# Performance work log

Measured on AMD Instinct MI355X. Metric: run time of the kernel, lower is better.

The kernel has to match this reference:

```python
import jax, jax.numpy as jnp
import numpy as np

KH, KW = 3, 3
C_OUT = 32


def setup_inputs() -> dict:
    key = jax.random.key(0)
    k1, k2, k3 = jax.random.split(key, 3)
    B, H, W, C_IN = 32, 128, 128, 32
    P_DIM = 128
    X = jax.random.normal(k1, (B, H, W, C_IN), dtype=jnp.float32)
    P = jax.random.normal(k2, (B, P_DIM), dtype=jnp.float32)
    # hypernetwork Dense weight: p_dim -> kh*kw*c_in*c_out (no bias, no activation)
    dense_w = jax.random.normal(k3, (P_DIM, KH * KW * C_IN * C_OUT), dtype=jnp.float32) * 0.05
    return {"X": X, "P": P, "dense_w": dense_w}


def _conv_one(x, w):
    # x: [H, W, c_in], w: [kh, kw, c_in, c_out] -> [H, W, c_out], SAME padding, stride 1
    y = jax.lax.conv_general_dilated(
        x[None], w, window_strides=(1, 1), padding="SAME",
        dimension_numbers=("NHWC", "HWIO", "NHWC"))
    return y[0]


def reference(X, P, dense_w):
    B = X.shape[0]
    c_in = X.shape[-1]
    # hypernetwork: per-sample conv kernels
    A = P @ dense_w                              # [B, kh*kw*c_in*c_out]
    Wk = A.reshape(B, KH, KW, c_in, C_OUT)       # [B, kh, kw, c_in, c_out]
    # batched per-sample conv (equivalent to tf.map_fn over conv2d)
    return jax.vmap(_conv_one)(X, Wk)            # [B, H, W, c_out]
```

## Files before the change

kernel.cpp:

```cpp
#include <hip/hip_runtime.h>


#define BATCH 32
#define HDIM 128
#define WDIM 128
#define CIN 32
#define COUT 32
#define PDIM 128
#define KCOLS 9216
#define XELEMS (BATCH * HDIM * WDIM * CIN)

typedef _Float16 f16x8 __attribute__((ext_vector_type(8)));
typedef float f32x4 __attribute__((ext_vector_type(4)));

__global__ __launch_bounds__(256) void prep_fused(const float* __restrict__ P,
                                                  const float* __restrict__ Dw,
                                                  const float* __restrict__ X,
                                                  unsigned short* __restrict__ WB,
                                                  f16x8* __restrict__ Xh8) {
    __shared__ float Pl[4 * PDIM];
    const int tid = threadIdx.x;

    if (blockIdx.x < 1152) {
        const int cg = blockIdx.x % 144;
        const int bg = blockIdx.x / 144;

        Pl[tid] = P[bg * 4 * PDIM + tid];
        Pl[tid + 256] = P[bg * 4 * PDIM + 256 + tid];
        __syncthreads();

        const int lane = tid & 63;
        const int wv = tid >> 6;
        const int col = cg * 64 + lane;
        const float* pw = &Pl[wv * PDIM];

        float acc = 0.f;
#pragma unroll 8
        for (int m = 0; m < PDIM; ++m) {
            acc += Dw[m * KCOLS + col] * pw[m];
        }

        const int k = col >> 5;
        const int co = col & 31;
        const int kc = k >> 5;
        const int ci = k & 31;
        const int base =
            ((kc * 2 + (co >> 4)) * 64 + (ci >> 3) * 16 + (co & 15)) * 8 + (ci & 7);
        const int b = bg * 4 + wv;
        _Float16 v = (_Float16)acc;
        WB[(size_t)b * KCOLS + base] = __builtin_bit_cast(unsigned short, v);
    } else {
        const int i0 = (blockIdx.x - 1152) * 256 + tid;
        if (i0 == 0) {
            f16x8 z;
#pragma unroll
            for (int j = 0; j < 8; ++j) z[j] = (_Float16)0.f;
            Xh8[-1] = z;
        }
        const f32x4* X4 = (const f32x4*)X;
#pragma unroll
        for (int r = 0; r < 4; ++r) {
            const int c = i0 + r * 524288;
            f32x4 a = X4[2 * c];
            f32x4 b = X4[2 * c + 1];
            f16x8 o;
#pragma unroll
            for (int j = 0; j < 4; ++j) {
                o[j] = (_Float16)a[j];
                o[4 + j] = (_Float16)b[j];
            }
            Xh8[c] = o;
        }
    }
}

__device__ __forceinline__ void load_tile(const f16x8* __restrict__ Xh8, int b,
                                          int h, int w0, int quad, int m16,
                                          f16x8 buf[9]) {
#pragma unroll
    for (int kc = 0; kc < 9; ++kc) {
        const int kh = kc / 3, kw = kc % 3;
        const int hh = h + kh - 1;
        const int ww = w0 + m16 + kw - 1;
        const bool ok = (hh >= 0) & (hh < HDIM) & (ww >= 0) & (ww < WDIM);
        int idx = ((b * HDIM + hh) * WDIM + ww) * 4 + quad;
        idx = ok ? idx : -1;
        buf[kc] = Xh8[idx];
    }
}

__global__ __launch_bounds__(256, 4) void cond_conv_f16(const f16x8* __restrict__ Xh8,
                                                        const unsigned short* __restrict__ WB,
                                                        float* __restrict__ Y) {
    __shared__ unsigned short WBl[KCOLS];
    const int tid = threadIdx.x;
    const int b = blockIdx.x >> 5;
    const int hg = blockIdx.x & 31;

    {
        const uint4* src = (const uint4*)(WB + (size_t)b * KCOLS);
        uint4* dst = (uint4*)WBl;
        for (int i = tid; i < KCOLS / 8; i += 256) dst[i] = src[i];
    }
    __syncthreads();

    const int wave = tid >> 6;
    const int lane = tid & 63;
    const int h = hg * 4 + wave;
    const int quad = lane >> 4;
    const int m16 = lane & 15;

    f16x8 bfrag[18];
#pragma unroll
    for (int i = 0; i < 18; ++i) {
        bfrag[i] = *(const f16x8*)(WBl + (i * 64 + lane) * 8);
    }

    f16x8 cur[9], nxt[9];
    load_tile(Xh8, b, h, 0, quad, m16, cur);

#pragma unroll
    for (int t = 0; t < 8; ++t) {
        if (t < 7) load_tile(Xh8, b, h, (t + 1) * 16, quad, m16, nxt);

        f32x4 acc0 = {0.f, 0.f, 0.f, 0.f};
        f32x4 acc1 = {0.f, 0.f, 0.f, 0.f};
#pragma unroll
        for (int kc = 0; kc < 9; ++kc) {
            acc0 = __builtin_amdgcn_mfma_f32_16x16x32_f16(cur[kc], bfrag[kc * 2], acc0, 0, 0, 0);
            acc1 = __builtin_amdgcn_mfma_f32_16x16x32_f16(cur[kc], bfrag[kc * 2 + 1], acc1, 0, 0, 0);
        }

        float* yp = Y + (((size_t)(b * HDIM + h) * WDIM) + t * 16 + quad * 4) * COUT + m16;
#pragma unroll
        for (int r = 0; r < 4; ++r) {
            yp[r * COUT] = acc0[r];
            yp[r * COUT + 16] = acc1[r];
        }

#pragma unroll
        for (int kc = 0; kc < 9; ++kc) cur[kc] = nxt[kc];
    }
}

__global__ __launch_bounds__(256, 4) void cond_conv_f32(const float* __restrict__ X,
                                                        const unsigned short* __restrict__ WB,
                                                        float* __restrict__ Y) {
    __shared__ unsigned short WBl[KCOLS];
    const int tid = threadIdx.x;
    const int b = blockIdx.x >> 5;
    const int hg = blockIdx.x & 31;
    {
        const uint4* src = (const uint4*)(WB + (size_t)b * KCOLS);
        uint4* dst = (uint4*)WBl;
        for (int i = tid; i < KCOLS / 8; i += 256) dst[i] = src[i];
    }
    __syncthreads();

    const int wave = tid >> 6;
    const int lane = tid & 63;
    const int h = hg * 4 + wave;
    const int quad = lane >> 4;
    const int m16 = lane & 15;
    const f32x4* X4 = (const f32x4*)X;

#pragma unroll 2
    for (int t = 0; t < 8; ++t) {
        const int w0 = t * 16;
        f32x4 acc0 = {0.f, 0.f, 0.f, 0.f};
        f32x4 acc1 = {0.f, 0.f, 0.f, 0.f};
#pragma unroll
        for (int kc = 0; kc < 9; ++kc) {
            const int kh = kc / 3, kw = kc % 3;
            const int hh = h + kh - 1;
            const int ww = w0 + m16 + kw - 1;
            const bool ok = (hh >= 0) & (hh < HDIM) & (ww >= 0) & (ww < WDIM);
            int idx = ((b * HDIM + hh) * WDIM + ww) * 8 + quad * 2;
            idx = ok ? idx : 0;
            f32x4 lo = X4[idx];
            f32x4 hi = X4[idx + 1];
            if (!ok) { lo = (f32x4)(0.f); hi = (f32x4)(0.f); }
            f16x8 a;
#pragma unroll
            for (int j = 0; j < 4; ++j) {
                a[j] = (_Float16)lo[j];
                a[4 + j] = (_Float16)hi[j];
            }
            const f16x8 bf0 = *(const f16x8*)(WBl + ((kc * 2 + 0) * 64 + lane) * 8);
            const f16x8 bf1 = *(const f16x8*)(WBl + ((kc * 2 + 1) * 64 + lane) * 8);
            acc0 = __builtin_amdgcn_mfma_f32_16x16x32_f16(a, bf0, acc0, 0, 0, 0);
            acc1 = __builtin_amdgcn_mfma_f32_16x16x32_f16(a, bf1, acc1, 0, 0, 0);
        }
        float* yp = Y + (((size_t)(b * HDIM + h) * WDIM) + w0 + quad * 4) * COUT + m16;
#pragma unroll
        for (int r = 0; r < 4; ++r) {
            yp[r * COUT] = acc0[r];
            yp[r * COUT + 16] = acc1[r];
        }
    }
}

extern "C" void kernel_launch(void* const* d_in, const int* in_sizes, int n_in,
                              void* d_out, int out_size, void* d_ws, size_t ws_size,
                              hipStream_t stream) {
    const float* X = (const float*)d_in[0];
    const float* P = (const float*)d_in[1];
    const float* Dw = (const float*)d_in[2];
    float* Y = (float*)d_out;

    unsigned short* WB = (unsigned short*)d_ws;
    const size_t need = (size_t)589824 + 64 + (size_t)XELEMS * 2;

    if (ws_size >= need) {
        f16x8* Xh8 = (f16x8*)((char*)d_ws + 589824 + 64);
        hipLaunchKernelGGL(prep_fused, dim3(1152 + 2048), dim3(256), 0, stream,
                           P, Dw, X, WB, Xh8);
        hipLaunchKernelGGL(cond_conv_f16, dim3(1024), dim3(256), 0, stream,
                           (const f16x8*)Xh8, WB, Y);
    } else {
        hipLaunchKernelGGL(prep_fused, dim3(1152), dim3(256), 0, stream,
                           P, Dw, X, WB, (f16x8*)nullptr);
        hipLaunchKernelGGL(cond_conv_f32, dim3(1024), dim3(256), 0, stream, X, WB, Y);
    }
}
```

Before: 149.0 us.

## Fuse X fp16 conversion into conv via LDS row tiles and rework hypernet GEMM

Drops the separate pass that converted X to fp16 in the workspace. The conv kernel now loads an 8-row fp32 tile of X per block, converts it to fp16, and stores it in a swizzled LDS buffer. Halo rows come from global memory and are prefetched per column tile, and weight fragments are read straight from global into registers. The hypernetwork GEMM now computes 8 batch rows per wave so each Dw load is reused, and blocks are remapped across batch and row-groups. This removes a full read and write of X in fp16, in exchange for a single GEMM launch of only 144 blocks and more complex LDS indexing.

```diff
diff --git a/kernel.cpp b/kernel.cpp
--- a/kernel.cpp
+++ b/kernel.cpp
@@ -8,130 +8,185 @@
 #define COUT 32
 #define PDIM 128
 #define KCOLS 9216
-#define XELEMS (BATCH * HDIM * WDIM * CIN)
 
 typedef _Float16 f16x8 __attribute__((ext_vector_type(8)));
 typedef float f32x4 __attribute__((ext_vector_type(4)));
 
-__global__ __launch_bounds__(256) void prep_fused(const float* __restrict__ P,
+__device__ __forceinline__ f16x8 zero8() {
+    f16x8 z;
+#pragma unroll
+    for (int j = 0; j < 8; ++j) z[j] = (_Float16)0.f;
+    return z;
+}
+
+__global__ __launch_bounds__(256) void hyper_gemm(const float* __restrict__ P,
                                                   const float* __restrict__ Dw,
-                                                  const float* __restrict__ X,
-                                                  unsigned short* __restrict__ WB,
-                                                  f16x8* __restrict__ Xh8) {
-    __shared__ float Pl[4 * PDIM];
+                                                  unsigned short* __restrict__ WB) {
     const int tid = threadIdx.x;
-
-    if (blockIdx.x < 1152) {
-        const int cg = blockIdx.x % 144;
-        const int bg = blockIdx.x / 144;
-
-        Pl[tid] = P[bg * 4 * PDIM + tid];
-        Pl[tid + 256] = P[bg * 4 * PDIM + 256 + tid];
-        __syncthreads();
-
-        const int lane = tid & 63;
-        const int wv = tid >> 6;
-        const int col = cg * 64 + lane;
-        const float* pw = &Pl[wv * PDIM];
-
-        float acc = 0.f;
-#pragma unroll 8
-        for (int m = 0; m < PDIM; ++m) {
-            acc += Dw[m * KCOLS + col] * pw[m];
-        }
-
-        const int k = col >> 5;
-        const int co = col & 31;
-        const int kc = k >> 5;
-        const int ci = k & 31;
-        const int base =
-            ((kc * 2 + (co >> 4)) * 64 + (ci >> 3) * 16 + (co & 15)) * 8 + (ci & 7);
-        const int b = bg * 4 + wv;
-        _Float16 v = (_Float16)acc;
-        WB[(size_t)b * KCOLS + base] = __builtin_bit_cast(unsigned short, v);
-    } else {
-        const int i0 = (blockIdx.x - 1152) * 256 + tid;
-        if (i0 == 0) {
-            f16x8 z;
-#pragma unroll
-            for (int j = 0; j < 8; ++j) z[j] = (_Float16)0.f;
-            Xh8[-1] = z;
-        }
-        const f32x4* X4 = (const f32x4*)X;
-#pragma unroll
-        for (int r = 0; r < 4; ++r) {
-            const int c = i0 + r * 524288;
-            f32x4 a = X4[2 * c];
-            f32x4 b = X4[2 * c + 1];
-            f16x8 o;
-#pragma unroll
-            for (int j = 0; j < 4; ++j) {
-                o[j] = (_Float16)a[j];
-                o[4 + j] = (_Float16)b[j];
-            }
-            Xh8[c] = o;
-        }
-    }
-}
-
-__device__ __forceinline__ void load_tile(const f16x8* __restrict__ Xh8, int b,
-                                          int h, int w0, int quad, int m16,
-                                          f16x8 buf[9]) {
-#pragma unroll
-    for (int kc = 0; kc < 9; ++kc) {
-        const int kh = kc / 3, kw = kc % 3;
-        const int hh = h + kh - 1;
-        const int ww = w0 + m16 + kw - 1;
-        const bool ok = (hh >= 0) & (hh < HDIM) & (ww >= 0) & (ww < WDIM);
-        int idx = ((b * HDIM + hh) * WDIM + ww) * 4 + quad;
-        idx = ok ? idx : -1;
-        buf[kc] = Xh8[idx];
-    }
-}
-
-__global__ __launch_bounds__(256, 4) void cond_conv_f16(const f16x8* __restrict__ Xh8,
-                                                        const unsigned short* __restrict__ WB,
-                                                        float* __restrict__ Y) {
-    __shared__ unsigned short WBl[KCOLS];
+    const int lane = tid & 63;
+    const int col = blockIdx.x * 64 + lane;
+    const int b0 = __builtin_amdgcn_readfirstlane((tid >> 6) * 8);
+    const float* pb = P + (size_t)b0 * PDIM;
+
+    float acc[8];
+#pragma unroll
+    for (int j = 0; j < 8; ++j) acc[j] = 0.f;
+
+#pragma unroll 2
+    for (int mm = 0; mm < PDIM; mm += 16) {
+        float d[16];
+#pragma unroll
+        for (int u = 0; u < 16; ++u) d[u] = Dw[(size_t)(mm + u) * KCOLS + col];
+#pragma unroll
+        for (int u = 0; u < 16; ++u) {
+#pragma unroll
+            for (int j = 0; j < 8; ++j) acc[j] += d[u] * pb[j * PDIM + mm + u];
+        }
+    }
+
+    const int co = col & 31;
+    const int k = col >> 5;
+    const int kc = k >> 5;
+    const int ci = k & 31;
+    const int base =
+        ((kc * 2 + (co >> 4)) * 64 + (ci >> 3) * 16 + (co & 15)) * 8 + (ci & 7);
+#pragma unroll
+    for (int j = 0; j < 8; ++j) {
+        _Float16 v = (_Float16)acc[j];
+        WB[(size_t)(b0 + j) * KCOLS + base] = __builtin_bit_cast(unsigned short, v);
+    }
+}
+
+__device__ __forceinline__ f16x8 halo_ld(const f32x4* __restrict__ gp, int px) {
+    const bool ok = (unsigned)px < 128u;
+    const int p = ok ? px : 0;
+    f32x4 lo = gp[p * 8];
+    f32x4 hi = gp[p * 8 + 1];
+    f16x8 o;
+#pragma unroll
+    for (int j = 0; j < 4; ++j) {
+        o[j] = (_Float16)lo[j];
+        o[4 + j] = (_Float16)hi[j];
+    }
+    if (!ok) o = zero8();
+    return o;
+}
+
+__global__ __launch_bounds__(512, 4) void conv_fused(const float* __restrict__ X,
+                                                     const unsigned short* __restrict__ WB,
+                                                     float* __restrict__ Y) {
+    __shared__ f16x8 Xs[8 * 512];
     const int tid = threadIdx.x;
-    const int b = blockIdx.x >> 5;
-    const int hg = blockIdx.x & 31;
-
-    {
-        const uint4* src = (const uint4*)(WB + (size_t)b * KCOLS);
-        uint4* dst = (uint4*)WBl;
-        for (int i = tid; i < KCOLS / 8; i += 256) dst[i] = src[i];
-    }
-    __syncthreads();
+
+    const int wg = blockIdx.x;
+    const int id = (wg & 7) * 64 + (wg >> 3);
+    const int b = id >> 4;
+    const int hg = id & 15;
+    const int r0 = hg * 8;
 
     const int wave = tid >> 6;
     const int lane = tid & 63;
-    const int h = hg * 4 + wave;
-    const int quad = lane >> 4;
+    const int q = lane >> 4;
     const int m16 = lane & 15;
 
-    f16x8 bfrag[18];
-#pragma unroll
-    for (int i = 0; i < 18; ++i) {
-        bfrag[i] = *(const f16x8*)(WBl + (i * 64 + lane) * 8);
-    }
-
-    f16x8 cur[9], nxt[9];
-    load_tile(Xh8, b, h, 0, quad, m16, cur);
+    f16x8 bf[18];
+    {
+        const f16x8* wbp = (const f16x8*)(WB + (size_t)b * KCOLS);
+#pragma unroll
+        for (int i = 0; i < 18; ++i) bf[i] = wbp[i * 64 + lane];
+    }
+
+    {
+        const int px_s = tid >> 2;
+        const int q_s = tid & 3;
+        const int g_s = px_s * 4 + ((q_s ^ (px_s >> 1)) & 3);
+        const float* xsrc =
+            X + (((size_t)b * HDIM + r0) * WDIM + px_s) * CIN + q_s * 8;
+#pragma unroll
+        for (int r = 0; r < 8; ++r) {
+            f32x4 lo = *(const f32x4*)(xsrc + (size_t)r * WDIM * CIN);
+            f32x4 hi = *(const f32x4*)(xsrc + (size_t)r * WDIM * CIN + 4);
+            f16x8 o;
+#pragma unroll
+            for (int j = 0; j < 4; ++j) {
+                o[j] = (_Float16)lo[j];
+                o[4 + j] = (_Float16)hi[j];
+            }
+            Xs[r * 512 + g_s] = o;
+        }
+    }
+
+    const bool top = (wave == 0);
+    const bool bot = (wave == 7);
+    const bool gvalid = top ? (hg != 0) : (bot ? (hg != 15) : false);
+    const int grow = top ? (r0 - 1) : (r0 + 8);
+    const f32x4* gp =
+        (const f32x4*)X + ((size_t)b * HDIM + (gvalid ? grow : 0)) * (WDIM * CIN / 4) +
+        q * 2;
+
+    f16x8 hal[3];
+    if (gvalid) {
+#pragma unroll
+        for (int kw = 0; kw < 3; ++kw) hal[kw] = halo_ld(gp, m16 + kw - 1);
+    } else {
+#pragma unroll
+        for (int kw = 0; kw < 3; ++kw) hal[kw] = zero8();
+    }
+
+    int va[3];
+#pragma unroll
+    for (int kw = 0; kw < 3; ++kw) {
+        const int px = m16 + kw - 1;
+        const int sl = (q ^ (px >> 1)) & 3;
+        va[kw] = (wave - 1) * 8192 + px * 64 + sl * 16;
+    }
+
+    __syncthreads();
+
+    const char* xsb = (const char*)Xs;
+    const int h = r0 + wave;
+    float* ybase = Y + (((size_t)b * HDIM + h) * WDIM + q * 4) * COUT + m16;
 
 #pragma unroll
     for (int t = 0; t < 8; ++t) {
-        if (t < 7) load_tile(Xh8, b, h, (t + 1) * 16, quad, m16, nxt);
-
         f32x4 acc0 = {0.f, 0.f, 0.f, 0.f};
         f32x4 acc1 = {0.f, 0.f, 0.f, 0.f};
-#pragma unroll
-        for (int kc = 0; kc < 9; ++kc) {
-            acc0 = __builtin_amdgcn_mfma_f32_16x16x32_f16(cur[kc], bfrag[kc * 2], acc0, 0, 0, 0);
-            acc1 = __builtin_amdgcn_mfma_f32_16x16x32_f16(cur[kc], bfrag[kc * 2 + 1], acc1, 0, 0, 0);
-        }
-
-        float* yp = Y + (((size_t)(b * HDIM + h) * WDIM) + t * 16 + quad * 4) * COUT + m16;
+
+#pragma unroll
+        for (int kh = 0; kh < 3; ++kh) {
+            f16x8 a0, a1, a2;
+            const bool use_lds =
+                (kh == 1) || (kh == 0 && wave != 0) || (kh == 2 && wave != 7);
+            if (use_lds) {
+                int v0 = va[0] + kh * 8192;
+                int v1 = va[1] + kh * 8192;
+                int v2 = va[2] + kh * 8192;
+                if (t == 0) v0 += (m16 == 0) ? 64 : 0;
+                if (t == 7) v2 -= (m16 == 15) ? 64 : 0;
+                a0 = *(const f16x8*)(xsb + v0);
+                a1 = *(const f16x8*)(xsb + v1);
+                a2 = *(const f16x8*)(xsb + v2);
+                if (t == 0 && m16 == 0) a0 = zero8();
+                if (t == 7 && m16 == 15) a2 = zero8();
+            } else {
+                a0 = hal[0];
+                a1 = hal[1];
+                a2 = hal[2];
+                if (gvalid && t < 7) {
+#pragma unroll
+                    for (int kw = 0; kw < 3; ++kw)
+                        hal[kw] = halo_ld(gp, (t + 1) * 16 + m16 + kw - 1);
+                }
+            }
+            acc0 = __builtin_amdgcn_mfma_f32_16x16x32_f16(a0, bf[(kh * 3 + 0) * 2], acc0, 0, 0, 0);
+            acc1 = __builtin_amdgcn_mfma_f32_16x16x32_f16(a0, bf[(kh * 3 + 0) * 2 + 1], acc1, 0, 0, 0);
+            acc0 = __builtin_amdgcn_mfma_f32_16x16x32_f16(a1, bf[(kh * 3 + 1) * 2], acc0, 0, 0, 0);
+            acc1 = __builtin_amdgcn_mfma_f32_16x16x32_f16(a1, bf[(kh * 3 + 1) * 2 + 1], acc1, 0, 0, 0);
+            acc0 = __builtin_amdgcn_mfma_f32_16x16x32_f16(a2, bf[(kh * 3 + 2) * 2], acc0, 0, 0, 0);
+            acc1 = __builtin_amdgcn_mfma_f32_16x16x32_f16(a2, bf[(kh * 3 + 2) * 2 + 1], acc1, 0, 0, 0);
+        }
+
+        float* yp = ybase + t * 16 * COUT;
 #pragma unroll
         for (int r = 0; r < 4; ++r) {
             yp[r * COUT] = acc0[r];
@@ -139,64 +194,7 @@
         }
 
 #pragma unroll
-        for (int kc = 0; kc < 9; ++kc) cur[kc] = nxt[kc];
-    }
-}
-
-__global__ __launch_bounds__(256, 4) void cond_conv_f32(const float* __restrict__ X,
-                                                        const unsigned short* __restrict__ WB,
-                                                        float* __restrict__ Y) {
-    __shared__ unsigned short WBl[KCOLS];
-    const int tid = threadIdx.x;
-    const int b = blockIdx.x >> 5;
-    const int hg = blockIdx.x & 31;
-    {
-        const uint4* src = (const uint4*)(WB + (size_t)b * KCOLS);
-        uint4* dst = (uint4*)WBl;
-        for (int i = tid; i < KCOLS / 8; i += 256) dst[i] = src[i];
-    }
-    __syncthreads();
-
-    const int wave = tid >> 6;
-    const int lane = tid & 63;
-    const int h = hg * 4 + wave;
-    const int quad = lane >> 4;
-    const int m16 = lane & 15;
-    const f32x4* X4 = (const f32x4*)X;
-
-#pragma unroll 2
-    for (int t = 0; t < 8; ++t) {
-        const int w0 = t * 16;
-        f32x4 acc0 = {0.f, 0.f, 0.f, 0.f};
-        f32x4 acc1 = {0.f, 0.f, 0.f, 0.f};
-#pragma unroll
-        for (int kc = 0; kc < 9; ++kc) {
-            const int kh = kc / 3, kw = kc % 3;
-            const int hh = h + kh - 1;
-            const int ww = w0 + m16 + kw - 1;
-            const bool ok = (hh >= 0) & (hh < HDIM) & (ww >= 0) & (ww < WDIM);
-            int idx = ((b * HDIM + hh) * WDIM + ww) * 8 + quad * 2;
-            idx = ok ? idx : 0;
-            f32x4 lo = X4[idx];
-            f32x4 hi = X4[idx + 1];
-            if (!ok) { lo = (f32x4)(0.f); hi = (f32x4)(0.f); }
-            f16x8 a;
-#pragma unroll
-            for (int j = 0; j < 4; ++j) {
-                a[j] = (_Float16)lo[j];
-                a[4 + j] = (_Float16)hi[j];
-            }
-            const f16x8 bf0 = *(const f16x8*)(WBl + ((kc * 2 + 0) * 64 + lane) * 8);
-            const f16x8 bf1 = *(const f16x8*)(WBl + ((kc * 2 + 1) * 64 + lane) * 8);
-            acc0 = __builtin_amdgcn_mfma_f32_16x16x32_f16(a, bf0, acc0, 0, 0, 0);
-            acc1 = __builtin_amdgcn_mfma_f32_16x16x32_f16(a, bf1, acc1, 0, 0, 0);
-        }
-        float* yp = Y + (((size_t)(b * HDIM + h) * WDIM) + w0 + quad * 4) * COUT + m16;
-#pragma unroll
-        for (int r = 0; r < 4; ++r) {
-            yp[r * COUT] = acc0[r];
-            yp[r * COUT + 16] = acc1[r];
-        }
+        for (int kw = 0; kw < 3; ++kw) va[kw] += 1024;
     }
 }
 
@@ -207,19 +205,11 @@
     const float* P = (const float*)d_in[1];
     const float* Dw = (const float*)d_in[2];
     float* Y = (float*)d_out;
+    (void)ws_size;
 
     unsigned short* WB = (unsigned short*)d_ws;
-    const size_t need = (size_t)589824 + 64 + (size_t)XELEMS * 2;
-
-    if (ws_size >= need) {
-        f16x8* Xh8 = (f16x8*)((char*)d_ws + 589824 + 64);
-        hipLaunchKernelGGL(prep_fused, dim3(1152 + 2048), dim3(256), 0, stream,
-                           P, Dw, X, WB, Xh8);
-        hipLaunchKernelGGL(cond_conv_f16, dim3(1024), dim3(256), 0, stream,
-                           (const f16x8*)Xh8, WB, Y);
-    } else {
-        hipLaunchKernelGGL(prep_fused, dim3(1152), dim3(256), 0, stream,
-                           P, Dw, X, WB, (f16x8*)nullptr);
-        hipLaunchKernelGGL(cond_conv_f32, dim3(1024), dim3(256), 0, stream, X, WB, Y);
-    }
-}
+
+    hipLaunchKernelGGL(hyper_gemm, dim3(144), dim3(256), 0, stream, P, Dw, WB);
+    hipLaunchKernelGGL(conv_fused, dim3(512), dim3(512), 0, stream,
+                       X, WB, Y);
+}
```

Result: no change. 150.8 us (+1.2%).
